# Optimization experiments

Hardware: AMD Instinct MI355X
Metric: run time of the kernel (lower is better)

Reference implementation:

```python
import jax, jax.numpy as jnp
import numpy as np

N_NODES = 100000
N_EDGES = 1600000
IN_FEATS, N_HIDDEN, N_CLASSES = 128, 64, 40


def setup_inputs() -> dict:
    key = jax.random.key(0)
    ks = jax.random.split(key, 6)
    h = jax.random.normal(ks[0], (N_NODES, IN_FEATS), dtype=jnp.float32)
    W0 = jax.random.normal(ks[1], (IN_FEATS, N_HIDDEN), dtype=jnp.float32) * (1.0 / np.sqrt(IN_FEATS))
    b0 = jnp.zeros((N_HIDDEN,), dtype=jnp.float32)
    W1 = jax.random.normal(ks[2], (N_HIDDEN, N_HIDDEN), dtype=jnp.float32) * (1.0 / np.sqrt(N_HIDDEN))
    b1 = jnp.zeros((N_HIDDEN,), dtype=jnp.float32)
    W2 = jax.random.normal(ks[3], (N_HIDDEN, N_CLASSES), dtype=jnp.float32) * (1.0 / np.sqrt(N_HIDDEN))
    b2 = jnp.zeros((N_CLASSES,), dtype=jnp.float32)
    src = jax.random.randint(ks[4], (N_EDGES,), 0, N_NODES, dtype=jnp.int32)
    dst = jax.random.randint(ks[5], (N_EDGES,), 0, N_NODES, dtype=jnp.int32)
    return {"h": h, "W0": W0, "b0": b0, "W1": W1, "b1": b1, "W2": W2, "b2": b2, "src": src, "dst": dst}


def _degrees(src, dst):
    ones = jnp.ones(src.shape[0], dtype=jnp.float32)
    out_deg = jax.ops.segment_sum(ones, src, num_segments=N_NODES)
    in_deg = jax.ops.segment_sum(ones, dst, num_segments=N_NODES)
    # DGL clamps degrees to >= 1 (allow_zero_in_degree)
    norm_src = jax.lax.rsqrt(jnp.maximum(out_deg, 1.0))  # [N]
    norm_dst = jax.lax.rsqrt(jnp.maximum(in_deg, 1.0))   # [N]
    return norm_src, norm_dst


def _graph_conv(x, W, b, src, dst, norm_src, norm_dst, act):
    # DGL GraphConv, norm='both': D_in^{-1/2} A^T D_out^{-1/2} (X W) + b
    xw = (x @ W) * norm_src[:, None]               # [N, out]
    agg = jax.ops.segment_sum(xw[src], dst, num_segments=N_NODES)  # gather-scatter over edges
    out = agg * norm_dst[:, None] + b
    return jax.nn.relu(out) if act else out


def reference(h, W0, b0, W1, b1, W2, b2, src, dst):
    norm_src, norm_dst = _degrees(src, dst)
    h = _graph_conv(h, W0, b0, src, dst, norm_src, norm_dst, act=True)
    # dropout layers are identity at inference
    h = _graph_conv(h, W1, b1, src, dst, norm_src, norm_dst, act=True)
    h = _graph_conv(h, W2, b2, src, dst, norm_src, norm_dst, act=False)
    return h
```

## Files before the change

kernel.cpp:

```cpp
#include <hip/hip_runtime.h>
#include <hip/hip_fp16.h>

#define N_NODES 100000
#define N_EDGES 1600000
#define ELL_W 64
#define ZROW N_NODES
#define NCHUNK 64
#define NSEG 4
#define CH (N_EDGES / NCHUNK)
#define SEGN (N_NODES / NSEG)
#define RDIV 25000u

typedef _Float16 half8 __attribute__((ext_vector_type(8)));
typedef float floatx4 __attribute__((ext_vector_type(4)));


__global__ __launch_bounds__(512) void k_count(const int* __restrict__ src, const int* __restrict__ dst,
                                               unsigned char* __restrict__ cnt_out,
                                               unsigned* __restrict__ cnt_in4) {
    __shared__ unsigned pkIn[SEGN];
    __shared__ unsigned pkOut[SEGN / 4];
    const int c = blockIdx.x;
    const int lo = blockIdx.y * SEGN;
    for (int i = threadIdx.x; i < SEGN; i += 512) pkIn[i] = 0;
    for (int i = threadIdx.x; i < SEGN / 4; i += 512) pkOut[i] = 0;
    __syncthreads();
    const int4* s4 = (const int4*)(src + c * CH);
    const int4* d4 = (const int4*)(dst + c * CH);
    for (int i = threadIdx.x; i < CH / 4; i += 512) {
        int4 s = s4[i], d = d4[i];
        unsigned a;
        a = (unsigned)(s.x - lo); if (a < SEGN) atomicAdd(&pkOut[a >> 2], 1u << ((a & 3) * 8));
        a = (unsigned)(s.y - lo); if (a < SEGN) atomicAdd(&pkOut[a >> 2], 1u << ((a & 3) * 8));
        a = (unsigned)(s.z - lo); if (a < SEGN) atomicAdd(&pkOut[a >> 2], 1u << ((a & 3) * 8));
        a = (unsigned)(s.w - lo); if (a < SEGN) atomicAdd(&pkOut[a >> 2], 1u << ((a & 3) * 8));
        a = (unsigned)(d.x - lo); if (a < SEGN) atomicAdd(&pkIn[a], 1u << (((unsigned)s.x / RDIV) * 8));
        a = (unsigned)(d.y - lo); if (a < SEGN) atomicAdd(&pkIn[a], 1u << (((unsigned)s.y / RDIV) * 8));
        a = (unsigned)(d.z - lo); if (a < SEGN) atomicAdd(&pkIn[a], 1u << (((unsigned)s.z / RDIV) * 8));
        a = (unsigned)(d.w - lo); if (a < SEGN) atomicAdd(&pkIn[a], 1u << (((unsigned)s.w / RDIV) * 8));
    }
    __syncthreads();
    for (int i = threadIdx.x; i < SEGN; i += 512) {
        cnt_in4[(size_t)c * N_NODES + lo + i] = pkIn[i];
        cnt_out[(size_t)c * N_NODES + lo + i] = (unsigned char)((pkOut[i >> 2] >> ((i & 3) * 8)) & 0xFF);
    }
}

__global__ __launch_bounds__(256) void k_scan(unsigned* __restrict__ cnt_in4,
                                              const unsigned char* __restrict__ cnt_out,
                                              int* __restrict__ fill, float* __restrict__ norm_src,
                                              float* __restrict__ norm_dst) {
    int d = blockIdx.x * 256 + threadIdx.x;
    if (d >= N_NODES) return;
    unsigned v[NCHUNK];
    unsigned dr0 = 0, dr1 = 0, dr2 = 0, dr3 = 0;
    #pragma unroll
    for (int c = 0; c < NCHUNK; ++c) {
        v[c] = cnt_in4[(size_t)c * N_NODES + d];
        dr0 += v[c] & 0xFF; dr1 += (v[c] >> 8) & 0xFF;
        dr2 += (v[c] >> 16) & 0xFF; dr3 += v[c] >> 24;
    }
    unsigned run = dr0 + dr1 + dr2 + dr3;
    unsigned roff = (dr0 << 8) | ((dr0 + dr1) << 16) | ((dr0 + dr1 + dr2) << 24);
    #pragma unroll
    for (int c = 0; c < NCHUNK; ++c) {
        cnt_in4[(size_t)c * N_NODES + d] = roff;
        roff += v[c];
    }
    int od = 0;
    for (int c = 0; c < NCHUNK; ++c) od += cnt_out[(size_t)c * N_NODES + d];
    fill[d] = (int)run;
    norm_dst[d] = rsqrtf((float)(run < 1 ? 1 : run));
    norm_src[d] = rsqrtf((float)(od  < 1 ? 1 : od ));
}

__global__ __launch_bounds__(512) void k_scatter(const int* __restrict__ src, const int* __restrict__ dst,
                                                 const unsigned* __restrict__ bases4,
                                                 int* __restrict__ ell) {
    __shared__ unsigned base4[SEGN];
    const int c = blockIdx.x;
    const int lo = blockIdx.y * SEGN;
    for (int i = threadIdx.x; i < SEGN; i += 512)
        base4[i] = bases4[(size_t)c * N_NODES + lo + i];
    __syncthreads();
    const int4* s4 = (const int4*)(src + c * CH);
    const int4* d4 = (const int4*)(dst + c * CH);
    for (int i = threadIdx.x; i < CH / 4; i += 512) {
        int4 s = s4[i], d = d4[i];
        unsigned r, sh, old; int p;
        r = (unsigned)(d.x - lo); if (r < SEGN) { sh = ((unsigned)s.x / RDIV) * 8; old = atomicAdd(&base4[r], 1u << sh); p = (old >> sh) & 0xFF; if (p < ELL_W) ell[p * N_NODES + lo + r] = s.x; }
        r = (unsigned)(d.y - lo); if (r < SEGN) { sh = ((unsigned)s.y / RDIV) * 8; old = atomicAdd(&base4[r], 1u << sh); p = (old >> sh) & 0xFF; if (p < ELL_W) ell[p * N_NODES + lo + r] = s.y; }
        r = (unsigned)(d.z - lo); if (r < SEGN) { sh = ((unsigned)s.z / RDIV) * 8; old = atomicAdd(&base4[r], 1u << sh); p = (old >> sh) & 0xFF; if (p < ELL_W) ell[p * N_NODES + lo + r] = s.z; }
        r = (unsigned)(d.w - lo); if (r < SEGN) { sh = ((unsigned)s.w / RDIV) * 8; old = atomicAdd(&base4[r], 1u << sh); p = (old >> sh) & 0xFF; if (p < ELL_W) ell[p * N_NODES + lo + r] = s.w; }
    }
}

__device__ __forceinline__ void acc16B(const float4& v, float* acc) {
    const __half2* hh = (const __half2*)&v;
    #pragma unroll
    for (int t = 0; t < 4; ++t) {
        float2 f = __half22float2(hh[t]);
        acc[2 * t + 0] += f.x;
        acc[2 * t + 1] += f.y;
    }
}

template<int KK>
__device__ __forceinline__ void loadb8(float4* V, const __half* __restrict__ base,
                                       const int* __restrict__ idxr, int b, int q) {
    #pragma unroll
    for (int u = 0; u < 8; ++u)
        V[u] = *(const float4*)(base + (long)idxr[b + u] * KK + q * 8);
}

__device__ __forceinline__ void accb8(const float4* V, float* acc) {
    #pragma unroll
    for (int u = 0; u < 8; ++u) acc16B(V[u], acc);
}

template<int KK>
__device__ __forceinline__ void gather_row(float* acc, const __half* __restrict__ XW,
                                           const int* __restrict__ idxr, int dg, int q) {
    int nb = (dg + 7) >> 3;
    if (nb <= 0) return;
    float4 va[8], vb[8];
    loadb8<KK>(va, XW, idxr, 0, q);
    int it = 1;
    for (; it + 1 < nb; it += 2) {
        loadb8<KK>(vb, XW, idxr, it * 8, q);
        accb8(va, acc);
        loadb8<KK>(va, XW, idxr, (it + 1) * 8, q);
        accb8(vb, acc);
    }
    if (it < nb) {
        loadb8<KK>(vb, XW, idxr, it * 8, q);
        accb8(va, acc);
        accb8(vb, acc);
    } else {
        accb8(va, acc);
    }
}

template<int K, int NCOL>
__global__ __launch_bounds__(256) void k_gemm(const float* __restrict__ Xv, const float* __restrict__ W,
                                              const float* __restrict__ norm, __half* __restrict__ Y,
                                              __half* __restrict__ padB, __half* __restrict__ padC) {
    constexpr int NT = (NCOL + 15) / 16;
    constexpr int NR = NT * 16;
    __shared__ __align__(16) _Float16 Xh[64][K + 8];
    __shared__ __align__(16) _Float16 Wt[NR][K + 8];
    const int tid = threadIdx.x;
    const int row0 = blockIdx.x * 64;

    if (blockIdx.x == 0) {
        if (tid < 32)       { ((unsigned*)(Y    + (size_t)N_NODES * 64))[tid]      = 0u; }
        else if (tid < 64)  { ((unsigned*)(padB + (size_t)N_NODES * 64))[tid - 32] = 0u; }
        else if (tid < 84)  { ((unsigned*)(padC + (size_t)N_NODES * 40))[tid - 64] = 0u; }
    }

    for (int idx = tid; idx < K * NCOL; idx += 256) {
        int k = idx / NCOL, c = idx - (idx / NCOL) * NCOL;
        Wt[c][k] = (_Float16)W[idx];
    }
    for (int idx = tid; idx < (NR - NCOL) * K; idx += 256) {
        int c = NCOL + idx / K, k = idx - (idx / K) * K;
        Wt[c][k] = (_Float16)0;
    }

    for (int idx = tid; idx < 64 * (K / 8); idx += 256) {
        int r = idx / (K / 8), kc = idx - (idx / (K / 8)) * (K / 8);
        int gr = row0 + r;
        half8 v = {0, 0, 0, 0, 0, 0, 0, 0};
        if (gr < N_NODES) {
            const float* X = Xv + (long)gr * K + kc * 8;
            float4 u0 = *(const float4*)(X + 0);
            float4 u1 = *(const float4*)(X + 4);
            v.s0 = (_Float16)u0.x; v.s1 = (_Float16)u0.y;
            v.s2 = (_Float16)u0.z; v.s3 = (_Float16)u0.w;
            v.s4 = (_Float16)u1.x; v.s5 = (_Float16)u1.y;
            v.s6 = (_Float16)u1.z; v.s7 = (_Float16)u1.w;
        }
        *(half8*)&Xh[r][kc * 8] = v;
    }
    __syncthreads();

    const int lane = tid & 63;
    const int wave = tid >> 6;
    const int quad = lane >> 4;
    const int l16 = lane & 15;
    const int r0 = wave * 16;

    floatx4 acc[NT] = {};
    #pragma unroll
    for (int k0 = 0; k0 < K; k0 += 32) {
        half8 a = *(const half8*)&Xh[r0 + l16][k0 + quad * 8];
        #pragma unroll
        for (int t = 0; t < NT; ++t) {
            half8 b = *(const half8*)&Wt[t * 16 + l16][k0 + quad * 8];
            acc[t] = __builtin_amdgcn_mfma_f32_16x16x32_f16(a, b, acc[t], 0, 0, 0);
        }
    }

    #pragma unroll
    for (int i = 0; i < 4; ++i) {
        int gr = row0 + r0 + quad * 4 + i;
        if (gr < N_NODES) {
            float s = norm[gr];
            #pragma unroll
            for (int t = 0; t < NT; ++t) {
                int c = t * 16 + l16;
                if (c < NCOL) Y[(long)gr * NCOL + c] = __float2half(acc[t][i] * s);
            }
        }
    }
}

template<int K, int NCOL>
__global__ __launch_bounds__(512, 4) void k_agg_gemm(const __half* __restrict__ XWp, const int* __restrict__ ell,
                                                     const int* __restrict__ deg, const float* __restrict__ norm_dst,
                                                     const float* __restrict__ biasp, const float* __restrict__ W,
                                                     const float* __restrict__ norm, __half* __restrict__ Y) {
    constexpr int NT = (NCOL + 15) / 16;
    constexpr int NR = NT * 16;
    __shared__ __align__(16) _Float16 Xh[64][K + 8];
    __shared__ __align__(16) _Float16 Wt[NR][K + 8];
    __shared__ int sIdx[64][68];
    __shared__ int sDeg[64];
    __shared__ int sMax;
    const int tid = threadIdx.x;
    const int row0 = blockIdx.x * 64;

    for (int idx = tid; idx < K * NCOL; idx += 512) {
        int k = idx / NCOL, c = idx - (idx / NCOL) * NCOL;
        Wt[c][k] = (_Float16)W[idx];
    }
    for (int idx = tid; idx < (NR - NCOL) * K; idx += 512) {
        int c = NCOL + idx / K, k = idx - (idx / K) * K;
        Wt[c][k] = (_Float16)0;
    }

    if (tid < 64) {
        int node = row0 + tid;
        int dg = 0;
        if (node < N_NODES) { dg = deg[node]; if (dg > ELL_W) dg = ELL_W; }
        sDeg[tid] = dg;
        int v = dg;
        #pragma unroll
        for (int o = 32; o > 0; o >>= 1) v = max(v, __shfl_down(v, o));
        if (tid == 0) sMax = v;
    }
    __syncthreads();
    const int mpad = (sMax + 7) & ~7;
    for (int i = tid; i < mpad * 64; i += 512) {
        int slot = i >> 6, r = i & 63;
        int node = row0 + r;
        sIdx[r][slot] = (node < N_NODES && slot < sDeg[r]) ? ell[slot * N_NODES + node] : ZROW;
    }
    __syncthreads();

    {
        int r = tid >> 3, q = tid & 7;
        int d = row0 + r;
        int dg = sDeg[r];
        const int* idxr = sIdx[r];
        float acc[8] = {};
        gather_row<K>(acc, XWp, idxr, dg, q);
        _Float16 res[8] = {};
        if (d < N_NODES) {
            float nd = norm_dst[d];
            #pragma unroll
            for (int t = 0; t < 8; ++t) {
                float o = acc[t] * nd + biasp[q * 8 + t];
                res[t] = (_Float16)fmaxf(o, 0.f);
            }
        }
        *(half8*)&Xh[r][q * 8] = *(const half8*)res;
    }
    __syncthreads();

    const int lane = tid & 63;
    const int wave = tid >> 6;
    if (wave < 4) {
        const int quad = lane >> 4;
        const int l16 = lane & 15;
        const int r0 = wave * 16;

        floatx4 acc[NT] = {};
        #pragma unroll
        for (int k0 = 0; k0 < K; k0 += 32) {
            half8 a = *(const half8*)&Xh[r0 + l16][k0 + quad * 8];
            #pragma unroll
            for (int t = 0; t < NT; ++t) {
                half8 b = *(const half8*)&Wt[t * 16 + l16][k0 + quad * 8];
                acc[t] = __builtin_amdgcn_mfma_f32_16x16x32_f16(a, b, acc[t], 0, 0, 0);
            }
        }

        #pragma unroll
        for (int i = 0; i < 4; ++i) {
            int gr = row0 + r0 + quad * 4 + i;
            if (gr < N_NODES) {
                float s = norm[gr];
                #pragma unroll
                for (int t = 0; t < NT; ++t) {
                    int c = t * 16 + l16;
                    if (c < NCOL) Y[(long)gr * NCOL + c] = __float2half(acc[t][i] * s);
                }
            }
        }
    }
}

template<int NF>
__global__ __launch_bounds__(320, 4) void k_agg_f(const __half* __restrict__ XW, const int* __restrict__ ell,
                                                  const int* __restrict__ deg, const float* __restrict__ norm_dst,
                                                  const float* __restrict__ bias, float* __restrict__ OUT) {
    constexpr int NQ = NF / 8;
    __shared__ int sIdx[64][68];
    __shared__ int sDeg[64];
    __shared__ int sMax;
    const int tid = threadIdx.x;
    const int row0 = blockIdx.x * 64;

    if (tid < 64) {
        int node = row0 + tid;
        int dg = 0;
        if (node < N_NODES) { dg = deg[node]; if (dg > ELL_W) dg = ELL_W; }
        sDeg[tid] = dg;
        int v = dg;
        #pragma unroll
        for (int o = 32; o > 0; o >>= 1) v = max(v, __shfl_down(v, o));
        if (tid == 0) sMax = v;
    }
    __syncthreads();
    const int mpad = (sMax + 7) & ~7;
    for (int i = tid; i < mpad * 64; i += 320) {
        int slot = i >> 6, r = i & 63;
        int node = row0 + r;
        sIdx[r][slot] = (node < N_NODES && slot < sDeg[r]) ? ell[slot * N_NODES + node] : ZROW;
    }
    __syncthreads();

    const int r = tid / NQ, q = tid - (tid / NQ) * NQ;
    const int d = row0 + r;
    if (d >= N_NODES) return;
    const int dg = sDeg[r];
    const int* idxr = sIdx[r];

    float acc[8] = {};
    gather_row<NF>(acc, XW, idxr, dg, q);

    float nd = norm_dst[d];
    float o[8];
    #pragma unroll
    for (int t = 0; t < 8; ++t) o[t] = acc[t] * nd + bias[q * 8 + t];
    *(float4*)(OUT + (long)d * NF + q * 8 + 0) = make_float4(o[0], o[1], o[2], o[3]);
    *(float4*)(OUT + (long)d * NF + q * 8 + 4) = make_float4(o[4], o[5], o[6], o[7]);
}

extern "C" void kernel_launch(void* const* d_in, const int* in_sizes, int n_in,
                              void* d_out, int out_size, void* d_ws, size_t ws_size,
                              hipStream_t stream) {
    const float* h  = (const float*)d_in[0];
    const float* W0 = (const float*)d_in[1];
    const float* b0 = (const float*)d_in[2];
    const float* W1 = (const float*)d_in[3];
    const float* b1 = (const float*)d_in[4];
    const float* W2 = (const float*)d_in[5];
    const float* b2 = (const float*)d_in[6];
    const int* src  = (const int*)d_in[7];
    const int* dst  = (const int*)d_in[8];
    float* out = (float*)d_out;

    char* ws = (char*)d_ws;
    size_t off = 0;
    int* fill        = (int*)(ws + off); off += (size_t)N_NODES * 4;
    float* norm_src  = (float*)(ws + off); off += (size_t)N_NODES * 4;
    float* norm_dst  = (float*)(ws + off); off += (size_t)N_NODES * 4;
    int* ell         = (int*)(ws + off); off += (size_t)N_NODES * ELL_W * 4;
    unsigned* cnt_in4 = (unsigned*)(ws + off);
    __half* bufA = (__half*)(ws + off);
    __half* bufC = (__half*)(ws + off + 13000000);
    off += (size_t)NCHUNK * N_NODES * 4;
    unsigned char* cnt_out = (unsigned char*)(ws + off); off += (size_t)NCHUNK * N_NODES;
    __half* bufB  = (__half*)(ws + off); off += (size_t)(N_NODES + 1) * 64 * 2;

    k_count<<<dim3(NCHUNK, NSEG), 512, 0, stream>>>(src, dst, cnt_out, cnt_in4);
    k_scan<<<(N_NODES + 255) / 256, 256, 0, stream>>>(cnt_in4, cnt_out, fill, norm_src, norm_dst);
    k_scatter<<<dim3(NCHUNK, NSEG), 512, 0, stream>>>(src, dst, cnt_in4, ell);

    const int grid = (N_NODES + 63) / 64;

    k_gemm<128, 64><<<grid, 256, 0, stream>>>(h, W0, norm_src, bufA, bufB, bufC);
    k_agg_gemm<64, 64><<<grid, 512, 0, stream>>>(bufA, ell, fill, norm_dst, b0, W1, norm_src, bufB);
    k_agg_gemm<64, 40><<<grid, 512, 0, stream>>>(bufB, ell, fill, norm_dst, b1, W2, norm_src, bufC);
    k_agg_f<40><<<grid, 320, 0, stream>>>(bufC, ell, fill, norm_dst, b2, out);
}
```

Baseline: 286.7 us.

## Replace src-range packed in-degree counters with byte counters over more chunks

The CSR/ELL build now counts in-degrees with byte-packed shared counters indexed by destination, instead of one 32-bit word per node split into four source-range sub-buckets. The grid becomes 128 chunks by 2 segments. This halves the per-chunk count arrays and lets the scan do a plain per-byte prefix sum, cutting preprocessing memory traffic and shared-memory footprint. The cost is that ELL rows are no longer grouped by source-index range, which may reduce gather locality in the three aggregation kernels.

```diff
diff --git a/kernel.cpp b/kernel.cpp
--- a/kernel.cpp
+++ b/kernel.cpp
@@ -5,11 +5,10 @@
 #define N_EDGES 1600000
 #define ELL_W 64
 #define ZROW N_NODES
-#define NCHUNK 64
-#define NSEG 4
+#define NCHUNK 128
+#define NSEG 2
 #define CH (N_EDGES / NCHUNK)
 #define SEGN (N_NODES / NSEG)
-#define RDIV 25000u
 
 typedef _Float16 half8 __attribute__((ext_vector_type(8)));
 typedef float floatx4 __attribute__((ext_vector_type(4)));
@@ -17,13 +16,12 @@
 
 __global__ __launch_bounds__(512) void k_count(const int* __restrict__ src, const int* __restrict__ dst,
                                                unsigned char* __restrict__ cnt_out,
-                                               unsigned* __restrict__ cnt_in4) {
-    __shared__ unsigned pkIn[SEGN];
+                                               unsigned char* __restrict__ cnt_in) {
+    __shared__ unsigned pkIn[SEGN / 4];
     __shared__ unsigned pkOut[SEGN / 4];
     const int c = blockIdx.x;
     const int lo = blockIdx.y * SEGN;
-    for (int i = threadIdx.x; i < SEGN; i += 512) pkIn[i] = 0;
-    for (int i = threadIdx.x; i < SEGN / 4; i += 512) pkOut[i] = 0;
+    for (int i = threadIdx.x; i < SEGN / 4; i += 512) { pkIn[i] = 0; pkOut[i] = 0; }
     __syncthreads();
     const int4* s4 = (const int4*)(src + c * CH);
     const int4* d4 = (const int4*)(dst + c * CH);
@@ -34,64 +32,54 @@
         a = (unsigned)(s.y - lo); if (a < SEGN) atomicAdd(&pkOut[a >> 2], 1u << ((a & 3) * 8));
         a = (unsigned)(s.z - lo); if (a < SEGN) atomicAdd(&pkOut[a >> 2], 1u << ((a & 3) * 8));
         a = (unsigned)(s.w - lo); if (a < SEGN) atomicAdd(&pkOut[a >> 2], 1u << ((a & 3) * 8));
-        a = (unsigned)(d.x - lo); if (a < SEGN) atomicAdd(&pkIn[a], 1u << (((unsigned)s.x / RDIV) * 8));
-        a = (unsigned)(d.y - lo); if (a < SEGN) atomicAdd(&pkIn[a], 1u << (((unsigned)s.y / RDIV) * 8));
-        a = (unsigned)(d.z - lo); if (a < SEGN) atomicAdd(&pkIn[a], 1u << (((unsigned)s.z / RDIV) * 8));
-        a = (unsigned)(d.w - lo); if (a < SEGN) atomicAdd(&pkIn[a], 1u << (((unsigned)s.w / RDIV) * 8));
-    }
-    __syncthreads();
-    for (int i = threadIdx.x; i < SEGN; i += 512) {
-        cnt_in4[(size_t)c * N_NODES + lo + i] = pkIn[i];
-        cnt_out[(size_t)c * N_NODES + lo + i] = (unsigned char)((pkOut[i >> 2] >> ((i & 3) * 8)) & 0xFF);
-    }
-}
-
-__global__ __launch_bounds__(256) void k_scan(unsigned* __restrict__ cnt_in4,
+        a = (unsigned)(d.x - lo); if (a < SEGN) atomicAdd(&pkIn[a >> 2], 1u << ((a & 3) * 8));
+        a = (unsigned)(d.y - lo); if (a < SEGN) atomicAdd(&pkIn[a >> 2], 1u << ((a & 3) * 8));
+        a = (unsigned)(d.z - lo); if (a < SEGN) atomicAdd(&pkIn[a >> 2], 1u << ((a & 3) * 8));
+        a = (unsigned)(d.w - lo); if (a < SEGN) atomicAdd(&pkIn[a >> 2], 1u << ((a & 3) * 8));
+    }
+    __syncthreads();
+    unsigned* win  = (unsigned*)(cnt_in  + (size_t)c * N_NODES + lo);
+    unsigned* wout = (unsigned*)(cnt_out + (size_t)c * N_NODES + lo);
+    for (int i = threadIdx.x; i < SEGN / 4; i += 512) { win[i] = pkIn[i]; wout[i] = pkOut[i]; }
+}
+
+__global__ __launch_bounds__(256) void k_scan(unsigned char* __restrict__ cnt_in,
                                               const unsigned char* __restrict__ cnt_out,
                                               int* __restrict__ fill, float* __restrict__ norm_src,
                                               float* __restrict__ norm_dst) {
     int d = blockIdx.x * 256 + threadIdx.x;
     if (d >= N_NODES) return;
-    unsigned v[NCHUNK];
-    unsigned dr0 = 0, dr1 = 0, dr2 = 0, dr3 = 0;
-    #pragma unroll
+    int run = 0;
     for (int c = 0; c < NCHUNK; ++c) {
-        v[c] = cnt_in4[(size_t)c * N_NODES + d];
-        dr0 += v[c] & 0xFF; dr1 += (v[c] >> 8) & 0xFF;
-        dr2 += (v[c] >> 16) & 0xFF; dr3 += v[c] >> 24;
-    }
-    unsigned run = dr0 + dr1 + dr2 + dr3;
-    unsigned roff = (dr0 << 8) | ((dr0 + dr1) << 16) | ((dr0 + dr1 + dr2) << 24);
-    #pragma unroll
-    for (int c = 0; c < NCHUNK; ++c) {
-        cnt_in4[(size_t)c * N_NODES + d] = roff;
-        roff += v[c];
+        int v = cnt_in[(size_t)c * N_NODES + d];
+        cnt_in[(size_t)c * N_NODES + d] = (unsigned char)run;
+        run += v;
     }
     int od = 0;
     for (int c = 0; c < NCHUNK; ++c) od += cnt_out[(size_t)c * N_NODES + d];
-    fill[d] = (int)run;
+    fill[d] = run;
     norm_dst[d] = rsqrtf((float)(run < 1 ? 1 : run));
     norm_src[d] = rsqrtf((float)(od  < 1 ? 1 : od ));
 }
 
 __global__ __launch_bounds__(512) void k_scatter(const int* __restrict__ src, const int* __restrict__ dst,
-                                                 const unsigned* __restrict__ bases4,
+                                                 const unsigned char* __restrict__ bases,
                                                  int* __restrict__ ell) {
-    __shared__ unsigned base4[SEGN];
+    __shared__ unsigned base4[SEGN / 4];
     const int c = blockIdx.x;
     const int lo = blockIdx.y * SEGN;
-    for (int i = threadIdx.x; i < SEGN; i += 512)
-        base4[i] = bases4[(size_t)c * N_NODES + lo + i];
+    const unsigned* bw = (const unsigned*)(bases + (size_t)c * N_NODES + lo);
+    for (int i = threadIdx.x; i < SEGN / 4; i += 512) base4[i] = bw[i];
     __syncthreads();
     const int4* s4 = (const int4*)(src + c * CH);
     const int4* d4 = (const int4*)(dst + c * CH);
     for (int i = threadIdx.x; i < CH / 4; i += 512) {
         int4 s = s4[i], d = d4[i];
         unsigned r, sh, old; int p;
-        r = (unsigned)(d.x - lo); if (r < SEGN) { sh = ((unsigned)s.x / RDIV) * 8; old = atomicAdd(&base4[r], 1u << sh); p = (old >> sh) & 0xFF; if (p < ELL_W) ell[p * N_NODES + lo + r] = s.x; }
-        r = (unsigned)(d.y - lo); if (r < SEGN) { sh = ((unsigned)s.y / RDIV) * 8; old = atomicAdd(&base4[r], 1u << sh); p = (old >> sh) & 0xFF; if (p < ELL_W) ell[p * N_NODES + lo + r] = s.y; }
-        r = (unsigned)(d.z - lo); if (r < SEGN) { sh = ((unsigned)s.z / RDIV) * 8; old = atomicAdd(&base4[r], 1u << sh); p = (old >> sh) & 0xFF; if (p < ELL_W) ell[p * N_NODES + lo + r] = s.z; }
-        r = (unsigned)(d.w - lo); if (r < SEGN) { sh = ((unsigned)s.w / RDIV) * 8; old = atomicAdd(&base4[r], 1u << sh); p = (old >> sh) & 0xFF; if (p < ELL_W) ell[p * N_NODES + lo + r] = s.w; }
+        r = (unsigned)(d.x - lo); if (r < SEGN) { sh = (r & 3) * 8; old = atomicAdd(&base4[r >> 2], 1u << sh); p = (old >> sh) & 0xFF; if (p < ELL_W) ell[p * N_NODES + lo + r] = s.x; }
+        r = (unsigned)(d.y - lo); if (r < SEGN) { sh = (r & 3) * 8; old = atomicAdd(&base4[r >> 2], 1u << sh); p = (old >> sh) & 0xFF; if (p < ELL_W) ell[p * N_NODES + lo + r] = s.y; }
+        r = (unsigned)(d.z - lo); if (r < SEGN) { sh = (r & 3) * 8; old = atomicAdd(&base4[r >> 2], 1u << sh); p = (old >> sh) & 0xFF; if (p < ELL_W) ell[p * N_NODES + lo + r] = s.z; }
+        r = (unsigned)(d.w - lo); if (r < SEGN) { sh = (r & 3) * 8; old = atomicAdd(&base4[r >> 2], 1u << sh); p = (old >> sh) & 0xFF; if (p < ELL_W) ell[p * N_NODES + lo + r] = s.w; }
     }
 }
 
@@ -378,16 +366,16 @@
     float* norm_src  = (float*)(ws + off); off += (size_t)N_NODES * 4;
     float* norm_dst  = (float*)(ws + off); off += (size_t)N_NODES * 4;
     int* ell         = (int*)(ws + off); off += (size_t)N_NODES * ELL_W * 4;
-    unsigned* cnt_in4 = (unsigned*)(ws + off);
+    unsigned char* cnt_in  = (unsigned char*)(ws + off);
     __half* bufA = (__half*)(ws + off);
     __half* bufC = (__half*)(ws + off + 13000000);
-    off += (size_t)NCHUNK * N_NODES * 4;
+    off += (size_t)NCHUNK * N_NODES;
     unsigned char* cnt_out = (unsigned char*)(ws + off); off += (size_t)NCHUNK * N_NODES;
     __half* bufB  = (__half*)(ws + off); off += (size_t)(N_NODES + 1) * 64 * 2;
 
-    k_count<<<dim3(NCHUNK, NSEG), 512, 0, stream>>>(src, dst, cnt_out, cnt_in4);
-    k_scan<<<(N_NODES + 255) / 256, 256, 0, stream>>>(cnt_in4, cnt_out, fill, norm_src, norm_dst);
-    k_scatter<<<dim3(NCHUNK, NSEG), 512, 0, stream>>>(src, dst, cnt_in4, ell);
+    k_count<<<dim3(NCHUNK, NSEG), 512, 0, stream>>>(src, dst, cnt_out, cnt_in);
+    k_scan<<<(N_NODES + 255) / 256, 256, 0, stream>>>(cnt_in, cnt_out, fill, norm_src, norm_dst);
+    k_scatter<<<dim3(NCHUNK, NSEG), 512, 0, stream>>>(src, dst, cnt_in, ell);
 
     const int grid = (N_NODES + 63) / 64;
 
```

New measurement: 278.9 us. 2.7% less time.
